# Kernel optimization log

Measured on AMD Instinct MI355X. Metric: run time of the kernel, lower is better.

The kernel has to match this reference:

```python
import jax, jax.numpy as jnp
import numpy as np

BATCH_SIZE = 2
EMBEDDING_DIM = 128
NUM_HEADS = 8
HEAD_DIM = EMBEDDING_DIM // NUM_HEADS  # 16
SEQ_LEN = 2048


def _split_heads(x, B, S):
    # Faithful to torch: reshape (B,S,head_dim,H) then transpose(2,3),(1,2)
    # -> (B,H,S,head_dim); head index is the fastest-varying dim of embedding.
    return x.reshape(B, S, HEAD_DIM, NUM_HEADS).transpose(0, 3, 1, 2)


def setup_inputs() -> dict:
    key = jax.random.key(0)
    k0, k1, k2, k3, k4 = jax.random.split(key, 5)
    inp = {
        "input_embeddings": jax.random.normal(k0, (BATCH_SIZE, SEQ_LEN, EMBEDDING_DIM), dtype=jnp.float32),
        "token_attention_masks_source": jax.random.randint(k1, (BATCH_SIZE, SEQ_LEN), 0, 2, dtype=jnp.int32),
        "token_attention_masks_target": jnp.ones((BATCH_SIZE, SEQ_LEN), dtype=jnp.int32),
        "masked": 0,  # encoder self-attention path (masked == False)
        # params: torch.rand -> uniform [0,1)
        "w_query": jax.random.uniform(k2, (EMBEDDING_DIM, EMBEDDING_DIM), dtype=jnp.float32),
        "w_key": jax.random.uniform(k3, (EMBEDDING_DIM, EMBEDDING_DIM), dtype=jnp.float32),
        "w_value": jax.random.uniform(k4, (EMBEDDING_DIM, EMBEDDING_DIM), dtype=jnp.float32),
    }
    return inp


def reference(input_embeddings, token_attention_masks_source, token_attention_masks_target, masked, w_query, w_key, w_value):
    B = BATCH_SIZE
    if not masked:
        S = token_attention_masks_source.shape[1]
    else:
        S = token_attention_masks_target.shape[1]

    # encoder_output_embedding is None in this path -> query from input_embeddings
    q = _split_heads(input_embeddings @ w_query, B, S)  # (B,H,S,hd)
    k = _split_heads(input_embeddings @ w_key, B, S)
    v = _split_heads(input_embeddings @ w_value, B, S)

    scale = jnp.einsum('bhqd,bhkd->bhqk', q, k) / jnp.sqrt(jnp.float32(HEAD_DIM))

    if not masked:
        # additive key mask: 0 -> -1000, 1 -> 0; broadcast over query dim
        add_mask = jnp.where(token_attention_masks_source == 0, jnp.float32(-1000.0), jnp.float32(0.0))
        scores = scale + add_mask[:, None, None, :]
    else:
        scores = scale

    probs = jax.nn.softmax(scores, axis=-1)
    ctx = jnp.einsum('bhqk,bhkd->bhqd', probs, v)  # (B,H,S,hd)
    # inverse of the split: (B,H,S,hd) -> (B,S,hd,H) -> (B,S,E)
    out = ctx.transpose(0, 2, 3, 1).reshape(B, S, HEAD_DIM * NUM_HEADS)
    return out
```

## Files before the change

kernel.cpp:

```cpp
#include <hip/hip_runtime.h>
#include <hip/hip_bf16.h>

#define B 2
#define S 2048
#define E 128
#define H 8
#define HD 16
#define BH (B*H)

#define RPB 8
#define KT 128

typedef __attribute__((ext_vector_type(8))) short bf16x8;
typedef __attribute__((ext_vector_type(4))) float f32x4;

__device__ __forceinline__ unsigned short f2b(float f) {
    const unsigned u = __float_as_uint(f);
    return (unsigned short)((u + 0x7FFFu + ((u >> 16) & 1u)) >> 16);
}
__device__ __forceinline__ float b2f(unsigned short u) {
    return __uint_as_float((unsigned)u << 16);
}

__global__ __launch_bounds__(64) void compact_idx(
    const int* __restrict__ mask, const int* __restrict__ masked_p,
    int* __restrict__ pos, int* __restrict__ cnt)
{
    const int b = blockIdx.x, lane = threadIdx.x;
    const int masked = *masked_p;
    int v[32];
    #pragma unroll
    for (int c = 0; c < 32; ++c)
        v[c] = mask[b * S + c * 64 + lane];

    int base = 0;
    #pragma unroll
    for (int c = 0; c < 32; ++c) {
        const bool keep = (masked != 0) || (v[c] != 0);
        const unsigned long long bal = __ballot(keep);
        const int my = base + (int)__popcll(bal & ((1ULL << lane) - 1ULL));
        pos[b * S + c * 64 + lane] = keep ? my : -1;
        base += (int)__popcll(bal);
    }
    if (base == 0) {
        #pragma unroll
        for (int c = 0; c < 32; ++c)
            pos[b * S + c * 64 + lane] = c * 64 + lane;
        base = S;
    }
    if (lane == 0) cnt[b] = base;
}

__global__ __launch_bounds__(64) void zero_tail(
    const int* __restrict__ cnt,
    unsigned short* __restrict__ Kxg, unsigned short* __restrict__ Btg)
{
    const int bh = blockIdx.x, b = bh >> 3;
    const int cn = cnt[b];
    const int pad = ((cn + KT - 1) / KT) * KT;
    const int nrows = pad - cn;
    unsigned short* KxB = Kxg + (size_t)bh * S * 32;
    unsigned short* BtB = Btg + (size_t)bh * S * 32;
    for (int idx = threadIdx.x; idx < nrows * 16; idx += 64) {
        const int row = cn + (idx >> 4), d = idx & 15;
        KxB[row * 32 + d]      = 0;
        KxB[row * 32 + 16 + d] = 0;
        BtB[((row >> 4) * 16 + d) * 32 + (row & 15)]      = 0;
        BtB[((row >> 4) * 16 + d) * 32 + (row & 15) + 16] = 0;
    }
}

__global__ __launch_bounds__(128) void qkv_proj(
    const float* __restrict__ x,
    const float* __restrict__ wq,
    const float* __restrict__ wk,
    const float* __restrict__ wv,
    const int* __restrict__ pos,
    float* __restrict__ Q,
    unsigned short* __restrict__ Kxg, unsigned short* __restrict__ Btg)
{
    __shared__ float xs[RPB][E];
    const int row0 = blockIdx.x * RPB;
    const int c    = threadIdx.x;
    #pragma unroll
    for (int rr = 0; rr < RPB; ++rr)
        xs[rr][c] = x[(size_t)(row0 + rr) * E + c];
    __syncthreads();

    float aq[RPB], ak[RPB], av[RPB];
    #pragma unroll
    for (int rr = 0; rr < RPB; ++rr) { aq[rr] = 0.f; ak[rr] = 0.f; av[rr] = 0.f; }

    for (int i = 0; i < E; ++i) {
        const float wqv = wq[i * E + c];
        const float wkv = wk[i * E + c];
        const float wvv = wv[i * E + c];
        #pragma unroll
        for (int rr = 0; rr < RPB; ++rr) {
            const float xv = xs[rr][i];
            aq[rr] = fmaf(xv, wqv, aq[rr]);
            ak[rr] = fmaf(xv, wkv, ak[rr]);
            av[rr] = fmaf(xv, wvv, av[rr]);
        }
    }

    const int h = c & 7, d = c >> 3;
    unsigned short* KxB = Kxg + (size_t)(0) ;
    #pragma unroll
    for (int rr = 0; rr < RPB; ++rr) {
        const int row = row0 + rr;
        const int b = row >> 11, s = row & 2047;
        const int bh = b * H + h;
        Q[(((size_t)bh) * S + s) * HD + d] = aq[rr] * 0.25f;
        const int p_ = pos[row];
        if (p_ >= 0) {
            const unsigned short kh = f2b(ak[rr]);
            const unsigned short kl = f2b(ak[rr] - b2f(kh));
            const unsigned short vh = f2b(av[rr]);
            const unsigned short vl = f2b(av[rr] - b2f(vh));
            unsigned short* kx = Kxg + (size_t)bh * S * 32 + (size_t)p_ * 32;
            kx[d]      = kh;
            kx[16 + d] = kl;
            unsigned short* bt = Btg + (size_t)bh * S * 32
                               + ((size_t)(p_ >> 4) * 16 + d) * 32 + (p_ & 15);
            bt[0]  = vh;
            bt[16] = vl;
        }
    }
    (void)KxB;
}

__global__ __launch_bounds__(128) void attn(
    const float* __restrict__ Q,
    const unsigned short* __restrict__ Kxg,
    const unsigned short* __restrict__ Btg,
    const int* __restrict__ cnt,
    float* __restrict__ out)
{
    const int bh    = blockIdx.y;
    const int b     = bh >> 3;
    const int h     = bh & 7;
    const int qtile = blockIdx.x;
    const int tid   = threadIdx.x;
    const int wid   = tid >> 6;
    const int lane  = tid & 63;
    const int col   = lane & 15;
    const int g     = lane >> 4;
    const int qrow0 = qtile * 32 + wid * 16;
    const int cn    = cnt[b];
    const int nt    = (cn + KT - 1) >> 7;

    const unsigned short* KxB = Kxg + (size_t)bh * S * 32;
    const unsigned short* BtB = Btg + (size_t)bh * S * 32;

    bf16x8 qh, ql;
    {
        const float* qp = Q + ((size_t)bh * S + qrow0 + col) * HD + 8 * (g & 1);
        #pragma unroll
        for (int i = 0; i < 8; ++i) {
            const float f = qp[i];
            const unsigned short hi = f2b(f);
            qh[i] = (short)hi;
            ql[i] = (short)f2b(f - b2f(hi));
        }
    }

    float m = -1e30f, l = 0.f;
    f32x4 acc = {0.f, 0.f, 0.f, 0.f};

    for (int kt = 0; kt < nt; ++kt) {
        const int base = kt * KT;

        f32x4 sc[8];
        #pragma unroll
        for (int kb = 0; kb < 8; ++kb) {
            const bf16x8 ka = *(const bf16x8*)(
                KxB + (size_t)(base + kb * 16 + col) * 32 + 8 * g);
            f32x4 c = {0.f, 0.f, 0.f, 0.f};
            c = __builtin_amdgcn_mfma_f32_16x16x32_bf16(ka, qh, c, 0, 0, 0);
            c = __builtin_amdgcn_mfma_f32_16x16x32_bf16(ka, ql, c, 0, 0, 0);
            sc[kb] = c;
        }
        if (base + KT > cn) {
            #pragma unroll
            for (int kb = 0; kb < 8; ++kb)
                #pragma unroll
                for (int r = 0; r < 4; ++r)
                    if (base + kb * 16 + 4 * g + r >= cn) sc[kb][r] = -1e30f;
        }

        float tm = sc[0][0];
        #pragma unroll
        for (int kb = 0; kb < 8; ++kb)
            #pragma unroll
            for (int r = 0; r < 4; ++r) tm = fmaxf(tm, sc[kb][r]);
        tm = fmaxf(tm, __shfl_xor(tm, 16));
        tm = fmaxf(tm, __shfl_xor(tm, 32));
        const float mn = fmaxf(m, tm);
        const float alpha = __expf(m - mn);
        m = mn;
        l *= alpha;
        #pragma unroll
        for (int r = 0; r < 4; ++r)
            acc[r] *= __shfl(alpha, 4 * g + r);

        #pragma unroll
        for (int kb = 0; kb < 8; ++kb) {
            const float p0 = __expf(sc[kb][0] - m);
            const float p1 = __expf(sc[kb][1] - m);
            const float p2 = __expf(sc[kb][2] - m);
            const float p3 = __expf(sc[kb][3] - m);
            float bl = p0 + p1 + p2 + p3;
            bl += __shfl_xor(bl, 16);
            bl += __shfl_xor(bl, 32);
            l += bl;

            const unsigned u01 = (unsigned)f2b(p0) | ((unsigned)f2b(p1) << 16);
            const unsigned u23 = (unsigned)f2b(p2) | ((unsigned)f2b(p3) << 16);
            const int s0 = col + 16 * (2 * (g & 1));
            const int s1 = s0 + 16;
            union { unsigned u[4]; bf16x8 v; } pa;
            pa.u[0] = (unsigned)__shfl((int)u01, s0);
            pa.u[1] = (unsigned)__shfl((int)u23, s0);
            pa.u[2] = (unsigned)__shfl((int)u01, s1);
            pa.u[3] = (unsigned)__shfl((int)u23, s1);

            const bf16x8 vb = *(const bf16x8*)(
                BtB + (size_t)((base >> 4) + kb) * 512 + col * 32 + 8 * g);
            acc = __builtin_amdgcn_mfma_f32_16x16x32_bf16(pa.v, vb, acc, 0, 0, 0);
        }
    }

    const float inv = 1.f / l;
    #pragma unroll
    for (int r = 0; r < 4; ++r) {
        const float ir = __shfl(inv, 4 * g + r);
        out[((size_t)(b * S + qrow0 + 4 * g + r)) * E + col * 8 + h] = acc[r] * ir;
    }
}

extern "C" void kernel_launch(void* const* d_in, const int* in_sizes, int n_in,
                              void* d_out, int out_size, void* d_ws, size_t ws_size,
                              hipStream_t stream) {
    int ix = 0, im0 = -1, isc = -1, iw[3] = {-1, -1, -1}, nw = 0;
    for (int i = 0; i < n_in; ++i) {
        const int sz = in_sizes[i];
        if (sz == B * S * E) ix = i;
        else if (sz == B * S) { if (im0 < 0) im0 = i; }
        else if (sz == E * E) { if (nw < 3) iw[nw++] = i; }
        else if (sz == 1 && isc < 0) isc = i;
    }
    if (im0 < 0) im0 = 1;
    if (isc < 0) isc = 3;
    if (nw < 3) { iw[0] = n_in - 3; iw[1] = n_in - 2; iw[2] = n_in - 1; }

    const float* x        = (const float*)d_in[ix];
    const int*   src_mask = (const int*)d_in[im0];
    const int*   masked_p = (const int*)d_in[isc];
    const float* wq       = (const float*)d_in[iw[0]];
    const float* wk       = (const float*)d_in[iw[1]];
    const float* wv       = (const float*)d_in[iw[2]];
    float*       out      = (float*)d_out;

    float*          Qw  = (float*)d_ws;
    unsigned short* Kxg = (unsigned short*)(Qw + (size_t)BH * S * HD);
    unsigned short* Btg = Kxg + (size_t)BH * S * 32;
    int*            pos = (int*)(Btg + (size_t)BH * S * 32);
    int*            cnt = pos + B * S;

    compact_idx<<<B, 64, 0, stream>>>(src_mask, masked_p, pos, cnt);
    zero_tail<<<BH, 64, 0, stream>>>(cnt, Kxg, Btg);
    qkv_proj<<<B * S / RPB, 128, 0, stream>>>(x, wq, wk, wv, pos, Qw, Kxg, Btg);
    attn<<<dim3(S / 32, BH), 128, 0, stream>>>(Qw, Kxg, Btg, cnt, out);
}
```

Measured before the change: 54.26 us.

## Split key range across two waves per query tile and merge with LDS

Each block now handles 16 query rows, and its two waves take alternating key tiles (split-K style). Partial max, sum and accumulator are merged through shared memory at the end. This doubles the grid and shortens each wave's serial loop. The change also skips the rescale step when no max increases, and defers the cross-lane row-sum reduction to the end of the loop. The cost is an extra LDS merge, a barrier, and duplicated Q loads across the two waves.

```diff
diff --git a/kernel.cpp b/kernel.cpp
--- a/kernel.cpp
+++ b/kernel.cpp
@@ -105,7 +105,6 @@
     }
 
     const int h = c & 7, d = c >> 3;
-    unsigned short* KxB = Kxg + (size_t)(0) ;
     #pragma unroll
     for (int rr = 0; rr < RPB; ++rr) {
         const int row = row0 + rr;
@@ -127,7 +126,6 @@
             bt[16] = vl;
         }
     }
-    (void)KxB;
 }
 
 __global__ __launch_bounds__(128) void attn(
@@ -137,16 +135,19 @@
     const int* __restrict__ cnt,
     float* __restrict__ out)
 {
+    __shared__ float Lm[16], Ll[16];
+    __shared__ f32x4 Lacc[64];
+
     const int bh    = blockIdx.y;
     const int b     = bh >> 3;
     const int h     = bh & 7;
-    const int qtile = blockIdx.x;
+    const int qg16  = blockIdx.x;
     const int tid   = threadIdx.x;
     const int wid   = tid >> 6;
     const int lane  = tid & 63;
     const int col   = lane & 15;
     const int g     = lane >> 4;
-    const int qrow0 = qtile * 32 + wid * 16;
+    const int qrow0 = qg16 * 16;
     const int cn    = cnt[b];
     const int nt    = (cn + KT - 1) >> 7;
 
@@ -168,7 +169,7 @@
     float m = -1e30f, l = 0.f;
     f32x4 acc = {0.f, 0.f, 0.f, 0.f};
 
-    for (int kt = 0; kt < nt; ++kt) {
+    for (int kt = wid; kt < nt; kt += 2) {
         const int base = kt * KT;
 
         f32x4 sc[8];
@@ -196,13 +197,15 @@
             for (int r = 0; r < 4; ++r) tm = fmaxf(tm, sc[kb][r]);
         tm = fmaxf(tm, __shfl_xor(tm, 16));
         tm = fmaxf(tm, __shfl_xor(tm, 32));
-        const float mn = fmaxf(m, tm);
-        const float alpha = __expf(m - mn);
-        m = mn;
-        l *= alpha;
-        #pragma unroll
-        for (int r = 0; r < 4; ++r)
-            acc[r] *= __shfl(alpha, 4 * g + r);
+        if (__any(tm > m)) {
+            const float mn = fmaxf(m, tm);
+            const float alpha = __expf(m - mn);
+            m = mn;
+            l *= alpha;
+            #pragma unroll
+            for (int r = 0; r < 4; ++r)
+                acc[r] *= __shfl(alpha, 4 * g + r);
+        }
 
         #pragma unroll
         for (int kb = 0; kb < 8; ++kb) {
@@ -210,10 +213,7 @@
             const float p1 = __expf(sc[kb][1] - m);
             const float p2 = __expf(sc[kb][2] - m);
             const float p3 = __expf(sc[kb][3] - m);
-            float bl = p0 + p1 + p2 + p3;
-            bl += __shfl_xor(bl, 16);
-            bl += __shfl_xor(bl, 32);
-            l += bl;
+            l += (p0 + p1) + (p2 + p3);
 
             const unsigned u01 = (unsigned)f2b(p0) | ((unsigned)f2b(p1) << 16);
             const unsigned u23 = (unsigned)f2b(p2) | ((unsigned)f2b(p3) << 16);
@@ -231,11 +231,31 @@
         }
     }
 
-    const float inv = 1.f / l;
-    #pragma unroll
-    for (int r = 0; r < 4; ++r) {
-        const float ir = __shfl(inv, 4 * g + r);
-        out[((size_t)(b * S + qrow0 + 4 * g + r)) * E + col * 8 + h] = acc[r] * ir;
+    l += __shfl_xor(l, 16);
+    l += __shfl_xor(l, 32);
+
+    if (wid == 1) {
+        if (g == 0) { Lm[col] = m; Ll[col] = l; }
+        Lacc[lane] = acc;
+    }
+    __syncthreads();
+    if (wid == 0) {
+        const float m1 = Lm[col];
+        const float l1 = Ll[col];
+        const f32x4 acc1 = Lacc[lane];
+        const float mn = fmaxf(m, m1);
+        const float a0 = __expf(m - mn);
+        const float a1 = __expf(m1 - mn);
+        const float ltot = l * a0 + l1 * a1;
+        const float inv = 1.f / ltot;
+        #pragma unroll
+        for (int r = 0; r < 4; ++r) {
+            const float b0 = __shfl(a0, 4 * g + r);
+            const float b1 = __shfl(a1, 4 * g + r);
+            const float ir = __shfl(inv, 4 * g + r);
+            const float v = (acc[r] * b0 + acc1[r] * b1) * ir;
+            out[((size_t)(b * S + qrow0 + 4 * g + r)) * E + col * 8 + h] = v;
+        }
     }
 }
 
@@ -271,5 +291,5 @@
     compact_idx<<<B, 64, 0, stream>>>(src_mask, masked_p, pos, cnt);
     zero_tail<<<BH, 64, 0, stream>>>(cnt, Kxg, Btg);
     qkv_proj<<<B * S / RPB, 128, 0, stream>>>(x, wq, wk, wv, pos, Qw, Kxg, Btg);
-    attn<<<dim3(S / 32, BH), 128, 0, stream>>>(Qw, Kxg, Btg, cnt, out);
-}
+    attn<<<dim3(S / 16, BH), 128, 0, stream>>>(Qw, Kxg, Btg, cnt, out);
+}
```

Result: slower. 60.17 us (+10.9%).

## Double-buffer K/V tiles in attention, defer row-sum reduction, merge prep kernels

Applied to the files above, without the earlier changes.

The attention loop now prefetches the next key tile's K and V fragments into registers while the current tile is computed, alternating between two register buffers. The cross-lane row-sum reduction moves out of the inner loop to a single reduction at the end. The running-max rescale is skipped when no lane's maximum changes. The mask compaction and tail-zeroing kernels are merged into one launch. Together these aim to hide global-load latency and cut shuffle and launch overhead, at the cost of higher register pressure that may lower occupancy.

```diff
diff --git a/kernel.cpp b/kernel.cpp
--- a/kernel.cpp
+++ b/kernel.cpp
@@ -22,12 +22,16 @@
     return __uint_as_float((unsigned)u << 16);
 }
 
-__global__ __launch_bounds__(64) void compact_idx(
+__global__ __launch_bounds__(64) void prep(
     const int* __restrict__ mask, const int* __restrict__ masked_p,
-    int* __restrict__ pos, int* __restrict__ cnt)
+    int* __restrict__ pos, int* __restrict__ cnt,
+    unsigned short* __restrict__ Kxg, unsigned short* __restrict__ Btg)
 {
-    const int b = blockIdx.x, lane = threadIdx.x;
+    const int bh = blockIdx.x;
+    const int b = bh >> 3, h = bh & 7;
+    const int lane = threadIdx.x;
     const int masked = *masked_p;
+
     int v[32];
     #pragma unroll
     for (int c = 0; c < 32; ++c)
@@ -38,30 +42,28 @@
     for (int c = 0; c < 32; ++c) {
         const bool keep = (masked != 0) || (v[c] != 0);
         const unsigned long long bal = __ballot(keep);
-        const int my = base + (int)__popcll(bal & ((1ULL << lane) - 1ULL));
-        pos[b * S + c * 64 + lane] = keep ? my : -1;
+        if (h == 0) {
+            const int my = base + (int)__popcll(bal & ((1ULL << lane) - 1ULL));
+            pos[b * S + c * 64 + lane] = keep ? my : -1;
+        }
         base += (int)__popcll(bal);
     }
-    if (base == 0) {
-        #pragma unroll
-        for (int c = 0; c < 32; ++c)
-            pos[b * S + c * 64 + lane] = c * 64 + lane;
-        base = S;
-    }
-    if (lane == 0) cnt[b] = base;
-}
-
-__global__ __launch_bounds__(64) void zero_tail(
-    const int* __restrict__ cnt,
-    unsigned short* __restrict__ Kxg, unsigned short* __restrict__ Btg)
-{
-    const int bh = blockIdx.x, b = bh >> 3;
-    const int cn = cnt[b];
+    int cn = base;
+    if (cn == 0) {
+        if (h == 0) {
+            #pragma unroll
+            for (int c = 0; c < 32; ++c)
+                pos[b * S + c * 64 + lane] = c * 64 + lane;
+        }
+        cn = S;
+    }
+    if (h == 0 && lane == 0) cnt[b] = cn;
+
     const int pad = ((cn + KT - 1) / KT) * KT;
     const int nrows = pad - cn;
     unsigned short* KxB = Kxg + (size_t)bh * S * 32;
     unsigned short* BtB = Btg + (size_t)bh * S * 32;
-    for (int idx = threadIdx.x; idx < nrows * 16; idx += 64) {
+    for (int idx = lane; idx < nrows * 16; idx += 64) {
         const int row = cn + (idx >> 4), d = idx & 15;
         KxB[row * 32 + d]      = 0;
         KxB[row * 32 + 16 + d] = 0;
@@ -105,7 +107,6 @@
     }
 
     const int h = c & 7, d = c >> 3;
-    unsigned short* KxB = Kxg + (size_t)(0) ;
     #pragma unroll
     for (int rr = 0; rr < RPB; ++rr) {
         const int row = row0 + rr;
@@ -127,7 +128,6 @@
             bt[16] = vl;
         }
     }
-    (void)KxB;
 }
 
 __global__ __launch_bounds__(128) void attn(
@@ -168,68 +168,87 @@
     float m = -1e30f, l = 0.f;
     f32x4 acc = {0.f, 0.f, 0.f, 0.f};
 
-    for (int kt = 0; kt < nt; ++kt) {
-        const int base = kt * KT;
-
-        f32x4 sc[8];
-        #pragma unroll
-        for (int kb = 0; kb < 8; ++kb) {
-            const bf16x8 ka = *(const bf16x8*)(
-                KxB + (size_t)(base + kb * 16 + col) * 32 + 8 * g);
-            f32x4 c = {0.f, 0.f, 0.f, 0.f};
-            c = __builtin_amdgcn_mfma_f32_16x16x32_bf16(ka, qh, c, 0, 0, 0);
-            c = __builtin_amdgcn_mfma_f32_16x16x32_bf16(ka, ql, c, 0, 0, 0);
-            sc[kb] = c;
-        }
-        if (base + KT > cn) {
-            #pragma unroll
-            for (int kb = 0; kb < 8; ++kb)
-                #pragma unroll
-                for (int r = 0; r < 4; ++r)
-                    if (base + kb * 16 + 4 * g + r >= cn) sc[kb][r] = -1e30f;
-        }
-
-        float tm = sc[0][0];
-        #pragma unroll
-        for (int kb = 0; kb < 8; ++kb)
-            #pragma unroll
-            for (int r = 0; r < 4; ++r) tm = fmaxf(tm, sc[kb][r]);
-        tm = fmaxf(tm, __shfl_xor(tm, 16));
-        tm = fmaxf(tm, __shfl_xor(tm, 32));
-        const float mn = fmaxf(m, tm);
-        const float alpha = __expf(m - mn);
-        m = mn;
-        l *= alpha;
-        #pragma unroll
-        for (int r = 0; r < 4; ++r)
-            acc[r] *= __shfl(alpha, 4 * g + r);
-
-        #pragma unroll
-        for (int kb = 0; kb < 8; ++kb) {
-            const float p0 = __expf(sc[kb][0] - m);
-            const float p1 = __expf(sc[kb][1] - m);
-            const float p2 = __expf(sc[kb][2] - m);
-            const float p3 = __expf(sc[kb][3] - m);
-            float bl = p0 + p1 + p2 + p3;
-            bl += __shfl_xor(bl, 16);
-            bl += __shfl_xor(bl, 32);
-            l += bl;
-
-            const unsigned u01 = (unsigned)f2b(p0) | ((unsigned)f2b(p1) << 16);
-            const unsigned u23 = (unsigned)f2b(p2) | ((unsigned)f2b(p3) << 16);
-            const int s0 = col + 16 * (2 * (g & 1));
-            const int s1 = s0 + 16;
-            union { unsigned u[4]; bf16x8 v; } pa;
-            pa.u[0] = (unsigned)__shfl((int)u01, s0);
-            pa.u[1] = (unsigned)__shfl((int)u23, s0);
-            pa.u[2] = (unsigned)__shfl((int)u01, s1);
-            pa.u[3] = (unsigned)__shfl((int)u23, s1);
-
-            const bf16x8 vb = *(const bf16x8*)(
-                BtB + (size_t)((base >> 4) + kb) * 512 + col * 32 + 8 * g);
-            acc = __builtin_amdgcn_mfma_f32_16x16x32_bf16(pa.v, vb, acc, 0, 0, 0);
-        }
-    }
+#define LOADT(KA, VB, TBASE)                                              \
+    {                                                                     \
+        const int base_ = (TBASE);                                        \
+        _Pragma("unroll")                                                 \
+        for (int kb = 0; kb < 8; ++kb) {                                  \
+            KA[kb] = *(const bf16x8*)(                                    \
+                KxB + (size_t)(base_ + kb * 16 + col) * 32 + 8 * g);      \
+            VB[kb] = *(const bf16x8*)(                                    \
+                BtB + (size_t)((base_ >> 4) + kb) * 512 + col * 32 + 8 * g); \
+        }                                                                 \
+    }
+
+#define COMPUTE(KA, VB, TBASE)                                            \
+    {                                                                     \
+        const int base_ = (TBASE);                                        \
+        f32x4 sc[8];                                                      \
+        _Pragma("unroll")                                                 \
+        for (int kb = 0; kb < 8; ++kb) {                                  \
+            f32x4 c_ = {0.f, 0.f, 0.f, 0.f};                              \
+            c_ = __builtin_amdgcn_mfma_f32_16x16x32_bf16(KA[kb], qh, c_, 0, 0, 0); \
+            c_ = __builtin_amdgcn_mfma_f32_16x16x32_bf16(KA[kb], ql, c_, 0, 0, 0); \
+            sc[kb] = c_;                                                  \
+        }                                                                 \
+        if (base_ + KT > cn) {                                            \
+            _Pragma("unroll")                                             \
+            for (int kb = 0; kb < 8; ++kb)                                \
+                _Pragma("unroll")                                         \
+                for (int r = 0; r < 4; ++r)                               \
+                    if (base_ + kb * 16 + 4 * g + r >= cn) sc[kb][r] = -1e30f; \
+        }                                                                 \
+        float tm = sc[0][0];                                              \
+        _Pragma("unroll")                                                 \
+        for (int kb = 0; kb < 8; ++kb)                                    \
+            _Pragma("unroll")                                             \
+            for (int r = 0; r < 4; ++r) tm = fmaxf(tm, sc[kb][r]);        \
+        tm = fmaxf(tm, __shfl_xor(tm, 16));                               \
+        tm = fmaxf(tm, __shfl_xor(tm, 32));                               \
+        if (__any(tm > m)) {                                              \
+            const float mn = fmaxf(m, tm);                                \
+            const float alpha = __expf(m - mn);                           \
+            m = mn;                                                       \
+            l *= alpha;                                                   \
+            _Pragma("unroll")                                             \
+            for (int r = 0; r < 4; ++r)                                   \
+                acc[r] *= __shfl(alpha, 4 * g + r);                       \
+        }                                                                 \
+        _Pragma("unroll")                                                 \
+        for (int kb = 0; kb < 8; ++kb) {                                  \
+            const float p0 = __expf(sc[kb][0] - m);                       \
+            const float p1 = __expf(sc[kb][1] - m);                       \
+            const float p2 = __expf(sc[kb][2] - m);                       \
+            const float p3 = __expf(sc[kb][3] - m);                       \
+            l += (p0 + p1) + (p2 + p3);                                   \
+            const unsigned u01 = (unsigned)f2b(p0) | ((unsigned)f2b(p1) << 16); \
+            const unsigned u23 = (unsigned)f2b(p2) | ((unsigned)f2b(p3) << 16); \
+            const int s0 = col + 16 * (2 * (g & 1));                      \
+            const int s1 = s0 + 16;                                       \
+            union { unsigned u[4]; bf16x8 v; } pa;                        \
+            pa.u[0] = (unsigned)__shfl((int)u01, s0);                     \
+            pa.u[1] = (unsigned)__shfl((int)u23, s0);                     \
+            pa.u[2] = (unsigned)__shfl((int)u01, s1);                     \
+            pa.u[3] = (unsigned)__shfl((int)u23, s1);                     \
+            acc = __builtin_amdgcn_mfma_f32_16x16x32_bf16(pa.v, VB[kb], acc, 0, 0, 0); \
+        }                                                                 \
+    }
+
+    bf16x8 kaA[8], vbA[8], kaB[8], vbB[8];
+    LOADT(kaA, vbA, 0);
+    for (int kt = 0; kt < nt; kt += 2) {
+        if (kt + 1 < nt) LOADT(kaB, vbB, (kt + 1) * KT);
+        COMPUTE(kaA, vbA, kt * KT);
+        if (kt + 1 < nt) {
+            if (kt + 2 < nt) LOADT(kaA, vbA, (kt + 2) * KT);
+            COMPUTE(kaB, vbB, (kt + 1) * KT);
+        }
+    }
+#undef LOADT
+#undef COMPUTE
+
+    l += __shfl_xor(l, 16);
+    l += __shfl_xor(l, 32);
 
     const float inv = 1.f / l;
     #pragma unroll
@@ -268,8 +287,7 @@
     int*            pos = (int*)(Btg + (size_t)BH * S * 32);
     int*            cnt = pos + B * S;
 
-    compact_idx<<<B, 64, 0, stream>>>(src_mask, masked_p, pos, cnt);
-    zero_tail<<<BH, 64, 0, stream>>>(cnt, Kxg, Btg);
+    prep<<<BH, 64, 0, stream>>>(src_mask, masked_p, pos, cnt, Kxg, Btg);
     qkv_proj<<<B * S / RPB, 128, 0, stream>>>(x, wq, wk, wv, pos, Qw, Kxg, Btg);
     attn<<<dim3(S / 32, BH), 128, 0, stream>>>(Qw, Kxg, Btg, cnt, out);
 }
```

After: 52.02 us. -4.1%, faster.
